# Kernel tuning notes

Measured on AMD Instinct MI355X. Metric: run time of the kernel, lower is better.

The kernel has to match this reference:

```python
import jax, jax.numpy as jnp
import numpy as np

EPS = 1e-12

def _normalize(v):
    n = jnp.linalg.norm(v, axis=-1, keepdims=True)
    return v / jnp.maximum(n, EPS)

def _bgs(J):
    # J: [b, N, D, 3, 2] -> rotation matrices R [b, N, D, 3, 3]
    b1 = _normalize(J[..., :, 0])
    a2 = J[..., :, 1]
    dot = jnp.sum(b1 * a2, axis=-1, keepdims=True)
    b2 = _normalize(a2 - dot * b1)
    b3 = jnp.cross(b1, b2)
    return jnp.stack([b1, b2, b3], axis=-1)  # columns b1,b2,b3

def setup_inputs() -> dict:
    key = jax.random.key(0)
    k1, k2, k3, k4, k5 = jax.random.split(key, 5)
    B, N, D, OUT = 16, 4096, 64, 64
    X = jax.random.normal(k1, (B, N, D, 3), dtype=jnp.float32)
    J = jax.random.normal(k2, (B, N, D, 3, 2), dtype=jnp.float32)
    A = jax.random.normal(k3, (OUT, D), dtype=jnp.float32)
    Bm = jax.random.normal(k4, (OUT, D), dtype=jnp.float32)
    C = jax.random.normal(k5, (OUT, D), dtype=jnp.float32)
    return {"X": X, "J": J, "A": A, "Bm": Bm, "C": C}

def reference(X, J, A, Bm, C):
    R = _bgs(J)  # [b, N, D, 3, 3]
    # RT_i . X == column i of R dotted with X -> scalar per channel
    RTX = jnp.einsum('bndij,bndi->bndj', R, X)  # [b, N, D, 3], j-th entry = RT_j X
    rt0 = RTX[..., 0:1]
    rt1 = RTX[..., 1:2]
    rt2 = RTX[..., 2:3]
    col0 = R[..., :, 0]
    col1 = R[..., :, 1]
    col2 = R[..., :, 2]
    # a_term (after adding b_term, as in original forward)
    a_term = col1 * rt1 + col2 * rt2 + col2 * rt1 - col1 * rt2  # [b, N, D, 3]
    c_term = col0 * rt0
    Y = jnp.einsum('fe,bnei->bnfi', A, a_term) + jnp.einsum('fe,bnei->bnfi', C, c_term)
    Y = jnp.einsum('fe,bnei->bnfi', Bm, Y)
    return Y
```

## Files before the change

### kernel.cpp

```cpp
#include <hip/hip_runtime.h>


typedef __bf16 bf16x8 __attribute__((ext_vector_type(8)));
typedef float floatx4 __attribute__((ext_vector_type(4)));

#define RSW 68
#define WLDS 2320

typedef const __attribute__((address_space(1))) unsigned guint;
typedef __attribute__((address_space(3))) unsigned suint;

static __device__ __forceinline__ void load16(const float* g, float* l) {
    __builtin_amdgcn_global_load_lds((guint*)g, (suint*)l, 16, 0, 0);
}

__global__ __launch_bounds__(256) void prep_kernel(const float* __restrict__ A,
                                                   const float* __restrict__ Bm,
                                                   const float* __restrict__ C,
                                                   __bf16* __restrict__ acat) {
    int tid = blockIdx.x * 256 + threadIdx.x;
    int f = tid >> 6;
    int e = tid & 63;
    float m = 0.f, m2 = 0.f;
    #pragma unroll 8
    for (int k = 0; k < 64; ++k) {
        float b = Bm[f * 64 + k];
        m  = fmaf(b, A[k * 64 + e], m);
        m2 = fmaf(b, C[k * 64 + e], m2);
    }
    acat[f * 128 + 2 * e]     = (__bf16)m;
    acat[f * 128 + 2 * e + 1] = (__bf16)m2;
}

static __device__ __forceinline__ unsigned pk(float a, float c) {
    unsigned short ua = __builtin_bit_cast(unsigned short, (__bf16)a);
    unsigned short uc = __builtin_bit_cast(unsigned short, (__bf16)c);
    return ((unsigned)uc << 16) | ua;
}

__global__ __launch_bounds__(256, 4) void main_kernel(const float* __restrict__ X,
                                                      const float* __restrict__ J,
                                                      const __bf16* __restrict__ acat,
                                                      float* __restrict__ out) {
    __shared__ __align__(16) float buf[4][WLDS];

    const int wave = threadIdx.x >> 6;
    const int lane = threadIdx.x & 63;
    const int l15  = lane & 15;
    const int quad = lane >> 4;
    float* stg = buf[wave];

    bf16x8 afrag[4][4];
    #pragma unroll
    for (int mt = 0; mt < 4; ++mt)
        #pragma unroll
        for (int kc = 0; kc < 4; ++kc)
            afrag[mt][kc] = *(const bf16x8*)(acat + (mt * 16 + l15) * 128 + kc * 32 + quad * 8);

    #pragma unroll 1
    for (int it = 0; it < 4; ++it) {
        const int tile = it * 4096 + blockIdx.x * 4 + wave;
        const size_t pbase = (size_t)tile * 4;

        const float* jg = J + pbase * 384;
        const float* xg = X + pbase * 192;
        #pragma unroll
        for (int t = 0; t < 6; ++t) load16(jg + (t * 64 + lane) * 4, stg + t * 256);
        #pragma unroll
        for (int t = 0; t < 3; ++t) load16(xg + (t * 64 + lane) * 4, stg + 1536 + t * 256);

        __asm__ volatile("s_waitcnt vmcnt(0)" ::: "memory");

        unsigned* zw = (unsigned*)stg;

        #pragma unroll
        for (int pi = 0; pi < 4; ++pi) {
            const float* jst = stg + pi * 384 + lane * 6;
            float2 ja = *(const float2*)(jst);
            float2 jb = *(const float2*)(jst + 2);
            float2 jc = *(const float2*)(jst + 4);
            const float* xst = stg + 1536 + pi * 192 + lane * 3;
            float xx = xst[0], xy = xst[1], xz = xst[2];

            float a0x = ja.x, a0y = jb.x, a0z = jc.x;
            float a1x = ja.y, a1y = jb.y, a1z = jc.y;

            float n0 = sqrtf(a0x * a0x + a0y * a0y + a0z * a0z);
            float r0 = 1.0f / fmaxf(n0, 1e-12f);
            float b1x = a0x * r0, b1y = a0y * r0, b1z = a0z * r0;

            float d  = b1x * a1x + b1y * a1y + b1z * a1z;
            float ux = a1x - d * b1x, uy = a1y - d * b1y, uz = a1z - d * b1z;
            float n2 = sqrtf(ux * ux + uy * uy + uz * uz);
            float r2 = 1.0f / fmaxf(n2, 1e-12f);
            float b2x = ux * r2, b2y = uy * r2, b2z = uz * r2;

            float b3x = b1y * b2z - b1z * b2y;
            float b3y = b1z * b2x - b1x * b2z;
            float b3z = b1x * b2y - b1y * b2x;

            float rt0 = b1x * xx + b1y * xy + b1z * xz;
            float rt1 = b2x * xx + b2y * xy + b2z * xz;
            float rt2 = b3x * xx + b3y * xy + b3z * xz;

            float s = rt1 - rt2, t = rt1 + rt2;

            unsigned* zr = zw + (pi * 3) * RSW;
            zr[lane]           = pk(b2x * s + b3x * t, b1x * rt0);
            zr[RSW + lane]     = pk(b2y * s + b3y * t, b1y * rt0);
            zr[2 * RSW + lane] = pk(b2z * s + b3z * t, b1z * rt0);
        }

        __asm__ volatile("s_waitcnt lgkmcnt(0)" ::: "memory");

        floatx4 acc[4];
        #pragma unroll
        for (int mt = 0; mt < 4; ++mt) acc[mt] = (floatx4){0.f, 0.f, 0.f, 0.f};

        int row = l15 > 11 ? 11 : l15;
        #pragma unroll
        for (int kc = 0; kc < 4; ++kc) {
            bf16x8 b = *(const bf16x8*)((const __bf16*)zw + row * 136 + kc * 32 + quad * 8);
            #pragma unroll
            for (int mt = 0; mt < 4; ++mt)
                acc[mt] = __builtin_amdgcn_mfma_f32_16x16x32_bf16(afrag[mt][kc], b, acc[mt], 0, 0, 0);
        }

        float* dl = stg + 832;
        #pragma unroll
        for (int mt = 0; mt < 4; ++mt) {
            int n = l15;
            if (n < 12) {
                int pl = (n * 21846) >> 16;
                int i  = n - pl * 3;
                float* dst = dl + pl * 196 + i;
                #pragma unroll
                for (int r = 0; r < 4; ++r) {
                    int f = mt * 16 + quad * 4 + r;
                    dst[f * 3] = acc[mt][r];
                }
            }
        }

        __asm__ volatile("s_waitcnt lgkmcnt(0)" ::: "memory");

        floatx4* og = (floatx4*)(out + pbase * 192);
        #pragma unroll
        for (int t = 0; t < 3; ++t) {
            int g  = t * 64 + lane;
            int pg = (g * 1366) >> 16;
            int o  = g - pg * 48;
            og[g] = *(const floatx4*)(dl + pg * 196 + o * 4);
        }
    }
}

extern "C" void kernel_launch(void* const* d_in, const int* in_sizes, int n_in,
                              void* d_out, int out_size, void* d_ws, size_t ws_size,
                              hipStream_t stream) {
    const float* X  = (const float*)d_in[0];
    const float* J  = (const float*)d_in[1];
    const float* A  = (const float*)d_in[2];
    const float* Bm = (const float*)d_in[3];
    const float* C  = (const float*)d_in[4];
    float* out = (float*)d_out;
    __bf16* acat = (__bf16*)d_ws;

    prep_kernel<<<16, 256, 0, stream>>>(A, Bm, C, acat);

    main_kernel<<<1024, 256, 0, stream>>>(X, J, acat, out);
}
```

Before: 212.9 us.

## Double-buffer J/X prefetch per wave and store MFMA results directly to global

Each wave now processes eight tiles with a two-slot LDS buffer for J, prefetching the next tile's J and X through global_load_lds while the current tile's MFMAs and stores run. The MFMA operands are swapped so the output is transposed, which lets results be written straight to global memory and removes the LDS staging pass and its extra wait. The grid is halved and launch bounds drop to two blocks per CU because of the larger LDS footprint. Occupancy falls, and the direct global stores are scalar and strided instead of coalesced 16-byte writes.

```diff
diff --git a/kernel.cpp b/kernel.cpp
--- a/kernel.cpp
+++ b/kernel.cpp
@@ -5,7 +5,7 @@
 typedef float floatx4 __attribute__((ext_vector_type(4)));
 
 #define RSW 68
-#define WLDS 2320
+#define ITERS 8
 
 typedef const __attribute__((address_space(1))) unsigned guint;
 typedef __attribute__((address_space(3))) unsigned suint;
@@ -38,52 +38,62 @@
     return ((unsigned)uc << 16) | ua;
 }
 
-__global__ __launch_bounds__(256, 4) void main_kernel(const float* __restrict__ X,
+__global__ __launch_bounds__(256, 2) void main_kernel(const float* __restrict__ X,
                                                       const float* __restrict__ J,
                                                       const __bf16* __restrict__ acat,
                                                       float* __restrict__ out) {
-    __shared__ __align__(16) float buf[4][WLDS];
+    __shared__ __align__(16) float buf[4][3840];
 
     const int wave = threadIdx.x >> 6;
     const int lane = threadIdx.x & 63;
     const int l15  = lane & 15;
     const int quad = lane >> 4;
     float* stg = buf[wave];
+    float* xb  = stg + 3072;
+
+    const int wid = blockIdx.x * 4 + wave;
 
     bf16x8 afrag[4][4];
     #pragma unroll
-    for (int mt = 0; mt < 4; ++mt)
+    for (int ft = 0; ft < 4; ++ft)
         #pragma unroll
         for (int kc = 0; kc < 4; ++kc)
-            afrag[mt][kc] = *(const bf16x8*)(acat + (mt * 16 + l15) * 128 + kc * 32 + quad * 8);
+            afrag[ft][kc] = *(const bf16x8*)(acat + (ft * 16 + l15) * 128 + kc * 32 + quad * 8);
 
-    #pragma unroll 1
-    for (int it = 0; it < 4; ++it) {
-        const int tile = it * 4096 + blockIdx.x * 4 + wave;
-        const size_t pbase = (size_t)tile * 4;
+    const int f3 = l15 * 3;
 
-        const float* jg = J + pbase * 384;
-        const float* xg = X + pbase * 192;
+    {
+        const size_t pb0 = (size_t)wid * 4;
+        const float* jg = J + pb0 * 384;
+        const float* xg = X + pb0 * 192;
         #pragma unroll
         for (int t = 0; t < 6; ++t) load16(jg + (t * 64 + lane) * 4, stg + t * 256);
         #pragma unroll
-        for (int t = 0; t < 3; ++t) load16(xg + (t * 64 + lane) * 4, stg + 1536 + t * 256);
+        for (int t = 0; t < 3; ++t) load16(xg + (t * 64 + lane) * 4, xb + t * 256);
+    }
+    __asm__ volatile("s_waitcnt vmcnt(0)" ::: "memory");
 
-        __asm__ volatile("s_waitcnt vmcnt(0)" ::: "memory");
+    #pragma unroll 1
+    for (int it = 0; it < ITERS; ++it) {
+        const int sel = it & 1;
+        float* jb = stg + sel * 1536;
+        const size_t pbase = ((size_t)it * 2048 + wid) * 4;
 
-        unsigned* zw = (unsigned*)stg;
+        __asm__ volatile("s_waitcnt vmcnt(16)" ::: "memory");
+
+        unsigned* zw = (unsigned*)jb;
 
         #pragma unroll
         for (int pi = 0; pi < 4; ++pi) {
-            const float* jst = stg + pi * 384 + lane * 6;
+            const float* jst = jb + pi * 384 + lane * 6;
             float2 ja = *(const float2*)(jst);
-            float2 jb = *(const float2*)(jst + 2);
+            float2 jbv = *(const float2*)(jst + 2);
             float2 jc = *(const float2*)(jst + 4);
-            const float* xst = stg + 1536 + pi * 192 + lane * 3;
+            const float* xst = xb + pi * 192 + lane * 3;
             float xx = xst[0], xy = xst[1], xz = xst[2];
 
-            float a0x = ja.x, a0y = jb.x, a0z = jc.x;
-            float a1x = ja.y, a1y = jb.y, a1z = jc.y;
+            float a0x = ja.x, a0y = jbv.x, a0z = jc.x;
+            float a1x = ja.y, a1y = jbv.y, a1z = jc.y;
 
             float n0 = sqrtf(a0x * a0x + a0y * a0y + a0z * a0z);
             float r0 = 1.0f / fmaxf(n0, 1e-12f);
@@ -111,46 +121,48 @@
             zr[2 * RSW + lane] = pk(b2z * s + b3z * t, b1z * rt0);
         }
 
+        if (it + 1 < ITERS) {
+            const size_t pbn = ((size_t)(it + 1) * 2048 + wid) * 4;
+            const float* jg = J + pbn * 384;
+            float* jbn = stg + (sel ^ 1) * 1536;
+            #pragma unroll
+            for (int t = 0; t < 6; ++t) load16(jg + (t * 64 + lane) * 4, jbn + t * 256);
+        }
+
         __asm__ volatile("s_waitcnt lgkmcnt(0)" ::: "memory");
+
+        if (it + 1 < ITERS) {
+            const size_t pbn = ((size_t)(it + 1) * 2048 + wid) * 4;
+            const float* xg = X + pbn * 192;
+            #pragma unroll
+            for (int t = 0; t < 3; ++t) load16(xg + (t * 64 + lane) * 4, xb + t * 256);
+        }
 
         floatx4 acc[4];
         #pragma unroll
-        for (int mt = 0; mt < 4; ++mt) acc[mt] = (floatx4){0.f, 0.f, 0.f, 0.f};
+        for (int ft = 0; ft < 4; ++ft) acc[ft] = (floatx4){0.f, 0.f, 0.f, 0.f};
 
         int row = l15 > 11 ? 11 : l15;
         #pragma unroll
         for (int kc = 0; kc < 4; ++kc) {
-            bf16x8 b = *(const bf16x8*)((const __bf16*)zw + row * 136 + kc * 32 + quad * 8);
+            bf16x8 zf = *(const bf16x8*)((const __bf16*)zw + row * 136 + kc * 32 + quad * 8);
             #pragma unroll
-            for (int mt = 0; mt < 4; ++mt)
-                acc[mt] = __builtin_amdgcn_mfma_f32_16x16x32_bf16(afrag[mt][kc], b, acc[mt], 0, 0, 0);
+            for (int ft = 0; ft < 4; ++ft)
+                acc[ft] = __builtin_amdgcn_mfma_f32_16x16x32_bf16(zf, afrag[ft][kc], acc[ft], 0, 0, 0);
         }
 
-        float* dl = stg + 832;
-        #pragma unroll
-        for (int mt = 0; mt < 4; ++mt) {
-            int n = l15;
-            if (n < 12) {
-                int pl = (n * 21846) >> 16;
+        if (quad < 3) {
+            float* base = out + pbase * 192 + f3;
+            #pragma unroll
+            for (int r = 0; r < 4; ++r) {
+                int n  = quad * 4 + r;
+                int pl = (n * 11) >> 5;
                 int i  = n - pl * 3;
-                float* dst = dl + pl * 196 + i;
+                float* dst = base + pl * 192 + i;
                 #pragma unroll
-                for (int r = 0; r < 4; ++r) {
-                    int f = mt * 16 + quad * 4 + r;
-                    dst[f * 3] = acc[mt][r];
-                }
+                for (int ft = 0; ft < 4; ++ft)
+                    dst[ft * 48] = acc[ft][r];
             }
-        }
-
-        __asm__ volatile("s_waitcnt lgkmcnt(0)" ::: "memory");
-
-        floatx4* og = (floatx4*)(out + pbase * 192);
-        #pragma unroll
-        for (int t = 0; t < 3; ++t) {
-            int g  = t * 64 + lane;
-            int pg = (g * 1366) >> 16;
-            int o  = g - pg * 48;
-            og[g] = *(const floatx4*)(dl + pg * 196 + o * 4);
         }
     }
 }
@@ -168,5 +180,5 @@
 
     prep_kernel<<<16, 256, 0, stream>>>(A, Bm, C, acat);
 
-    main_kernel<<<1024, 256, 0, stream>>>(X, J, acat, out);
+    main_kernel<<<512, 256, 0, stream>>>(X, J, acat, out);
 }
```

New measurement: 211.3 us. Within noise of the previous version (-0.7%).
